# Performance work log

Measured on AMD Instinct MI355X. Metric: run time of the kernel, lower is better.

## Reference

```python
import jax, jax.numpy as jnp
import numpy as np

DIVERSITY_WEIGHT = 0.3
UNCERTAINTY_WEIGHT = 0.3
EPS_NORM = 1e-12  # torch F.normalize eps
EPS_LOG = 1e-8


def setup_inputs() -> dict:
    key = jax.random.key(0)
    k1, k2 = jax.random.split(key)
    B, N, D, C = 8, 8192, 512, 2
    x = jax.random.normal(k1, (B, N, D), dtype=jnp.float32)
    c = jax.random.normal(k2, (B, N, C), dtype=jnp.float32)
    return {"x": x, "c": c, "big_lambda": 512}


def reference(x, c, big_lambda):
    B, N, D = x.shape
    C = c.shape[-1]
    big_lambda = min(big_lambda, N)

    # relevance: max class score per instance (C > 1 branch)
    if C == 1:
        relevance = c[..., 0]
    else:
        relevance = jnp.max(c, axis=-1)  # [B, N]

    # diversity: 1 - mean cosine similarity to all other patches.
    # Row-sum of the N x N cosine-sim matrix factorizes:
    #   sum_j xn_i . xn_j = xn_i . (sum_j xn_j)  -> O(N*D) instead of O(N^2*D)
    norms = jnp.linalg.norm(x, axis=-1, keepdims=True)
    x_norm = x / jnp.maximum(norms, EPS_NORM)          # [B, N, D]
    s = jnp.sum(x_norm, axis=1)                        # [B, D]
    row_sums = jnp.einsum('bnd,bd->bn', x_norm, s)     # [B, N]
    avg_sim = (row_sums - 1.0) / (N - 1)
    diversity = 1.0 - avg_sim

    # uncertainty: entropy of class distribution
    if C == 1:
        p = jax.nn.sigmoid(c[..., 0])
        probs = jnp.stack([1.0 - p, p], axis=-1)
    else:
        probs = jax.nn.softmax(c, axis=-1)
    uncertainty = -jnp.sum(probs * jnp.log(probs + EPS_LOG), axis=-1)  # [B, N]

    combined = relevance + DIVERSITY_WEIGHT * diversity + UNCERTAINTY_WEIGHT * uncertainty

    _, selected_indices = jax.lax.top_k(combined, big_lambda)  # [B, big_lambda]
    attention_weights = jax.nn.softmax(combined, axis=1)       # [B, N]
    return selected_indices, attention_weights
```

## Files before the change

### kernel.cpp

```cpp
#include <hip/hip_runtime.h>
#include <stdint.h>

#define B 8
#define N 8192
#define D 512
#define K 512
#define DIV_W 0.3f
#define UNC_W 0.3f

constexpr int ROWS_PER_WAVE  = 16;
constexpr int WAVES_PER_BLK  = 4;
constexpr int ROWS_PER_BLOCK = ROWS_PER_WAVE * WAVES_PER_BLK;
constexpr int BLOCKS_PER_B   = N / ROWS_PER_BLOCK;

constexpr float DIVC = DIV_W * (1.0f + 1.0f / 8191.0f);
constexpr float COEF = DIV_W / 8191.0f;

__device__ __forceinline__ uint32_t ordmap(float f) {
    uint32_t u = __float_as_uint(f);
    return (u & 0x80000000u) ? ~u : (u | 0x80000000u);
}
__device__ __forceinline__ float ordunmap(uint32_t u) {
    return (u >> 31) ? __uint_as_float(u & 0x7FFFFFFFu) : __uint_as_float(~u);
}

__global__ __launch_bounds__(256) void k_norm_s(const float* __restrict__ x,
                                                const float* __restrict__ c,
                                                float* __restrict__ inv_norm,
                                                float* __restrict__ partials,
                                                float* __restrict__ combined) {
    int blk  = blockIdx.x;
    int b    = blk / BLOCKS_PER_B;
    int rb   = (blk % BLOCKS_PER_B) * ROWS_PER_BLOCK;
    int tid  = threadIdx.x;
    int wave = tid >> 6;
    int lane = tid & 63;

    const float4* xb = (const float4*)(x + (size_t)b * N * D);

    float4 accA = {0.f, 0.f, 0.f, 0.f};
    float4 accB = {0.f, 0.f, 0.f, 0.f};

    int row0 = rb + wave * ROWS_PER_WAVE;
    #pragma unroll 4
    for (int r = 0; r < ROWS_PER_WAVE; ++r) {
        int row = row0 + r;
        const float4* xr = xb + (size_t)row * (D / 4);
        float4 a  = xr[lane];
        float4 bb = xr[64 + lane];

        float ss = a.x*a.x + a.y*a.y + a.z*a.z + a.w*a.w
                 + bb.x*bb.x + bb.y*bb.y + bb.z*bb.z + bb.w*bb.w;
        #pragma unroll
        for (int o = 32; o > 0; o >>= 1) ss += __shfl_xor(ss, o, 64);

        float inv = 1.0f / fmaxf(sqrtf(ss), 1e-12f);
        if (lane == 0) inv_norm[b * N + row] = inv;

        accA.x += a.x * inv;  accA.y += a.y * inv;
        accA.z += a.z * inv;  accA.w += a.w * inv;
        accB.x += bb.x * inv; accB.y += bb.y * inv;
        accB.z += bb.z * inv; accB.w += bb.w * inv;
    }

    if (lane < 16) {
        int row = row0 + lane;
        float2 cv = ((const float2*)c)[(size_t)b * N + row];
        float rel = fmaxf(cv.x, cv.y);
        float e0 = expf(cv.x - rel), e1 = expf(cv.y - rel);
        float Z  = e0 + e1;
        float p0 = e0 / Z, p1 = e1 / Z;
        float ent = -(p0 * logf(p0 + 1e-8f) + p1 * logf(p1 + 1e-8f));
        combined[b * N + row] = rel + UNC_W * ent + DIVC;
    }

    __shared__ float sp[WAVES_PER_BLK][D];
    float* dA = &sp[wave][lane * 4];
    dA[0] = accA.x; dA[1] = accA.y; dA[2] = accA.z; dA[3] = accA.w;
    float* dB = &sp[wave][256 + lane * 4];
    dB[0] = accB.x; dB[1] = accB.y; dB[2] = accB.z; dB[3] = accB.w;
    __syncthreads();

    float* dst = partials + (size_t)blk * D;
    for (int d = tid; d < D; d += 256)
        dst[d] = sp[0][d] + sp[1][d] + sp[2][d] + sp[3][d];
}

__global__ __launch_bounds__(512) void k_reduce_s(const float* __restrict__ partials,
                                                  float* __restrict__ s) {
    int b = blockIdx.x;
    int d = threadIdx.x;
    const float* p = partials + (size_t)b * BLOCKS_PER_B * D + d;
    float acc = 0.f;
    #pragma unroll 16
    for (int j = 0; j < BLOCKS_PER_B; ++j) acc += p[(size_t)j * D];
    s[b * D + d] = acc;
}

__global__ __launch_bounds__(256) void k_combined(const float* __restrict__ x,
                                                  const float* __restrict__ inv_norm,
                                                  const float* __restrict__ s,
                                                  float* __restrict__ combined) {
    __shared__ float sl[D];
    int blk  = blockIdx.x;
    int b    = blk / BLOCKS_PER_B;
    int rb   = (blk % BLOCKS_PER_B) * ROWS_PER_BLOCK;
    int tid  = threadIdx.x;
    int wave = tid >> 6;
    int lane = tid & 63;

    for (int d = tid; d < D; d += 256) sl[d] = s[b * D + d];
    __syncthreads();

    const float4* sv = (const float4*)sl;
    float4 sA = sv[lane];
    float4 sB = sv[64 + lane];

    const float4* xb = (const float4*)(x + (size_t)b * N * D);
    int row0 = rb + wave * ROWS_PER_WAVE;
    #pragma unroll 4
    for (int r = 0; r < ROWS_PER_WAVE; ++r) {
        int row = row0 + r;
        const float4* xr = xb + (size_t)row * (D / 4);
        float4 a  = xr[lane];
        float4 bb = xr[64 + lane];

        float dot = a.x*sA.x + a.y*sA.y + a.z*sA.z + a.w*sA.w
                  + bb.x*sB.x + bb.y*sB.y + bb.z*sB.z + bb.w*sB.w;
        #pragma unroll
        for (int o = 32; o > 0; o >>= 1) dot += __shfl_xor(dot, o, 64);

        if (lane == 0) {
            float rs = dot * inv_norm[b * N + row];
            combined[b * N + row] -= COEF * rs;
        }
    }
}

struct P3 {
    unsigned long long cand[K];
    uint32_t hist[256];
    uint32_t tiew[256];
    uint16_t rnk[2][K];
    uint32_t wred[16];
    float    fred[16];
    uint32_t sc_prefix, sc_remK, sc_cnt;
};

__global__ __launch_bounds__(1024) void k_topk_sm(const float* __restrict__ combined,
                                                  float* __restrict__ out_idx,
                                                  float* __restrict__ out_w) {
    __shared__ P3 p3;

    const int b    = blockIdx.x;
    const int tid  = threadIdx.x;
    const int lane = tid & 63;
    const int wave = tid >> 6;

    const float4* cb4 = (const float4*)(combined + b * N);
    float4 f0 = cb4[tid];
    float4 f1 = cb4[1024 + tid];

    uint32_t v[8];
    v[0] = ordmap(f0.x); v[1] = ordmap(f0.y); v[2] = ordmap(f0.z); v[3] = ordmap(f0.w);
    v[4] = ordmap(f1.x); v[5] = ordmap(f1.y); v[6] = ordmap(f1.z); v[7] = ordmap(f1.w);

    uint32_t umax = 0;
    #pragma unroll
    for (int q = 0; q < 8; ++q) umax = max(umax, v[q]);
    #pragma unroll
    for (int o = 32; o > 0; o >>= 1) umax = max(umax, __shfl_xor(umax, o, 64));
    if (lane == 0) p3.wred[wave] = umax;
    if (tid == 0) { p3.sc_remK = K; p3.sc_prefix = 0u; p3.sc_cnt = 0u; }
    __syncthreads();
    uint32_t bmax = p3.wred[0];
    #pragma unroll
    for (int q = 1; q < 16; ++q) bmax = max(bmax, p3.wred[q]);
    const float m = ordunmap(bmax);

    float e[8];
    float sum = 0.f;
    #pragma unroll
    for (int q = 0; q < 8; ++q) { e[q] = expf(ordunmap(v[q]) - m); sum += e[q]; }
    #pragma unroll
    for (int o = 32; o > 0; o >>= 1) sum += __shfl_xor(sum, o, 64);
    if (lane == 0) p3.fred[wave] = sum;
    __syncthreads();
    float Z = 0.f;
    #pragma unroll
    for (int q = 0; q < 16; ++q) Z += p3.fred[q];
    const float invZ = 1.0f / Z;
    float4* ow = (float4*)(out_w + b * N);
    float4 w0 = {e[0]*invZ, e[1]*invZ, e[2]*invZ, e[3]*invZ};
    float4 w1 = {e[4]*invZ, e[5]*invZ, e[6]*invZ, e[7]*invZ};
    ow[tid]        = w0;
    ow[1024 + tid] = w1;

    uint32_t prefix = 0, maskHi = 0;
    for (int p = 3; p >= 0; --p) {
        if (tid < 256) p3.hist[tid] = 0u;
        __syncthreads();
        const int sh = 8 * p;
        if (p == 3) {
            #pragma unroll
            for (int q = 0; q < 8; ++q) {
                uint32_t bin = v[q] >> 24;
                bool pred = true;
                unsigned long long todo = ~0ULL;
                while (todo) {
                    int leader = __ffsll(todo) - 1;
                    uint32_t lbin = __shfl(bin, leader, 64);
                    unsigned long long same = __ballot(pred && (bin == lbin));
                    if (lane == leader) atomicAdd(&p3.hist[lbin], (uint32_t)__popcll(same));
                    todo &= ~same;
                    if (bin == lbin) pred = false;
                }
            }
        } else {
            #pragma unroll
            for (int q = 0; q < 8; ++q) {
                if ((v[q] & maskHi) == prefix)
                    atomicAdd(&p3.hist[(v[q] >> sh) & 0xFFu], 1u);
            }
        }
        __syncthreads();
        if (wave == 0) {
            uint32_t cc[4], lsum = 0;
            #pragma unroll
            for (int q = 0; q < 4; ++q) { cc[q] = p3.hist[lane * 4 + q]; lsum += cc[q]; }
            uint32_t ssum = lsum;
            #pragma unroll
            for (int off = 1; off < 64; off <<= 1) {
                uint32_t t2 = __shfl_down(ssum, off, 64);
                if (lane + off < 64) ssum += t2;
            }
            uint32_t cum = ssum - lsum;
            const uint32_t remK = p3.sc_remK;
            #pragma unroll
            for (int q = 3; q >= 0; --q) {
                if (cum < remK && cum + cc[q] >= remK) {
                    p3.sc_prefix = prefix | ((uint32_t)(lane * 4 + q) << sh);
                    p3.sc_remK   = remK - cum;
                }
                cum += cc[q];
            }
        }
        __syncthreads();
        prefix = p3.sc_prefix;
        maskHi |= (0xFFu << sh);
    }
    const uint32_t T    = prefix;
    const uint32_t remF = p3.sc_remK;

    if (tid < 256) p3.tiew[tid] = 0u;
    __syncthreads();
    #pragma unroll
    for (int q = 0; q < 8; ++q) {
        uint32_t idx = (q < 4) ? (uint32_t)(4 * tid + q)
                               : (uint32_t)(4096 + 4 * tid + (q - 4));
        bool g = (v[q] > T);
        unsigned long long mask = __ballot(g);
        if (mask) {
            int leader = __ffsll(mask) - 1;
            uint32_t bcnt = (uint32_t)__popcll(mask);
            uint32_t wbase = 0;
            if (lane == leader) wbase = atomicAdd(&p3.sc_cnt, bcnt);
            wbase = __shfl(wbase, leader, 64);
            if (g) {
                uint32_t off = (uint32_t)__popcll(mask & ((1ULL << lane) - 1ULL));
                p3.cand[wbase + off] = ((uint64_t)v[q] << 13) | (uint32_t)(8191 - idx);
            }
        }
        if (v[q] == T) atomicOr(&p3.tiew[idx >> 5], 1u << (idx & 31));
    }
    __syncthreads();
    const uint32_t base = p3.sc_cnt;
    if (wave == 0) {
        const int w0i = lane * 4;
        uint32_t lsum = 0;
        #pragma unroll
        for (int q = 0; q < 4; ++q) lsum += __popc(p3.tiew[w0i + q]);
        uint32_t ssum = lsum;
        #pragma unroll
        for (int off = 1; off < 64; off <<= 1) {
            uint32_t t2 = __shfl_up(ssum, off, 64);
            if (lane >= off) ssum += t2;
        }
        uint32_t rank = ssum - lsum;
        for (int q = 0; q < 4; ++q) {
            uint32_t word = p3.tiew[w0i + q];
            while (word) {
                int bpos = __builtin_ctz(word);
                if (rank < remF) {
                    uint32_t idx = (uint32_t)(w0i + q) * 32u + (uint32_t)bpos;
                    p3.cand[base + rank] = ((uint64_t)T << 13) | (uint32_t)(8191 - idx);
                }
                rank++;
                word &= word - 1;
            }
        }
    }
    __syncthreads();

    {
        const int ki   = tid & 511;
        const int half = tid >> 9;
        const uint64_t me = p3.cand[ki];
        const int j0 = half * 256;
        uint32_t cnt = 0;
        #pragma unroll 8
        for (int j = 0; j < 256; ++j)
            cnt += (p3.cand[j0 + j] > me) ? 1u : 0u;
        p3.rnk[half][ki] = (uint16_t)cnt;
    }
    __syncthreads();
    if (tid < K) {
        uint32_t rank = (uint32_t)p3.rnk[0][tid] + (uint32_t)p3.rnk[1][tid];
        uint32_t idx  = 8191u - (uint32_t)(p3.cand[tid] & 0x1FFFu);
        out_idx[b * K + rank] = (float)idx;
    }
}

extern "C" void kernel_launch(void* const* d_in, const int* in_sizes, int n_in,
                              void* d_out, int out_size, void* d_ws, size_t ws_size,
                              hipStream_t stream) {
    const float* x = (const float*)d_in[0];
    const float* c = (const float*)d_in[1];

    float* ws       = (float*)d_ws;
    float* partials = ws;
    float* s        = partials + B * BLOCKS_PER_B * D;
    float* inv_norm = s + B * D;
    float* combined = inv_norm + B * N;

    float* out = (float*)d_out;

    k_norm_s  <<<B * BLOCKS_PER_B, 256, 0, stream>>>(x, c, inv_norm, partials, combined);
    k_reduce_s<<<B, 512, 0, stream>>>(partials, s);
    k_combined<<<B * BLOCKS_PER_B, 256, 0, stream>>>(x, inv_norm, s, combined);
    k_topk_sm <<<B, 1024, 0, stream>>>(combined, out, out + B * K);
}
```

Before: 81.31 us.

## Replace partial-sum reduce kernel with atomics and rank-count with bitonic sort

Each norm block now adds its per-block column sums into s with atomicAdd, which removes the separate k_reduce_s launch and the partials buffer, but adds a memset. In the top-k kernel, the O(K^2) rank counting over candidates is replaced by a 512-element bitonic sort that uses shuffles for small strides and shared memory for large ones. The softmax exponent also switches to __expf. Float atomics make the accumulation order nondeterministic, and __expf gives slightly less precise weights.

```diff
diff --git a/kernel.cpp b/kernel.cpp
--- a/kernel.cpp
+++ b/kernel.cpp
@@ -27,7 +27,7 @@
 __global__ __launch_bounds__(256) void k_norm_s(const float* __restrict__ x,
                                                 const float* __restrict__ c,
                                                 float* __restrict__ inv_norm,
-                                                float* __restrict__ partials,
+                                                float* __restrict__ s,
                                                 float* __restrict__ combined) {
     int blk  = blockIdx.x;
     int b    = blk / BLOCKS_PER_B;
@@ -81,20 +81,10 @@
     dB[0] = accB.x; dB[1] = accB.y; dB[2] = accB.z; dB[3] = accB.w;
     __syncthreads();
 
-    float* dst = partials + (size_t)blk * D;
-    for (int d = tid; d < D; d += 256)
-        dst[d] = sp[0][d] + sp[1][d] + sp[2][d] + sp[3][d];
-}
-
-__global__ __launch_bounds__(512) void k_reduce_s(const float* __restrict__ partials,
-                                                  float* __restrict__ s) {
-    int b = blockIdx.x;
-    int d = threadIdx.x;
-    const float* p = partials + (size_t)b * BLOCKS_PER_B * D + d;
-    float acc = 0.f;
-    #pragma unroll 16
-    for (int j = 0; j < BLOCKS_PER_B; ++j) acc += p[(size_t)j * D];
-    s[b * D + d] = acc;
+    for (int d = tid; d < D; d += 256) {
+        float v = sp[0][d] + sp[1][d] + sp[2][d] + sp[3][d];
+        atomicAdd(&s[b * D + d], v);
+    }
 }
 
 __global__ __launch_bounds__(256) void k_combined(const float* __restrict__ x,
@@ -141,7 +131,6 @@
     unsigned long long cand[K];
     uint32_t hist[256];
     uint32_t tiew[256];
-    uint16_t rnk[2][K];
     uint32_t wred[16];
     float    fred[16];
     uint32_t sc_prefix, sc_remK, sc_cnt;
@@ -181,7 +170,7 @@
     float e[8];
     float sum = 0.f;
     #pragma unroll
-    for (int q = 0; q < 8; ++q) { e[q] = expf(ordunmap(v[q]) - m); sum += e[q]; }
+    for (int q = 0; q < 8; ++q) { e[q] = __expf(ordunmap(v[q]) - m); sum += e[q]; }
     #pragma unroll
     for (int o = 32; o > 0; o >>= 1) sum += __shfl_xor(sum, o, 64);
     if (lane == 0) p3.fred[wave] = sum;
@@ -302,23 +291,27 @@
     }
     __syncthreads();
 
-    {
-        const int ki   = tid & 511;
-        const int half = tid >> 9;
-        const uint64_t me = p3.cand[ki];
-        const int j0 = half * 256;
-        uint32_t cnt = 0;
-        #pragma unroll 8
-        for (int j = 0; j < 256; ++j)
-            cnt += (p3.cand[j0 + j] > me) ? 1u : 0u;
-        p3.rnk[half][ki] = (uint16_t)cnt;
-    }
-    __syncthreads();
-    if (tid < K) {
-        uint32_t rank = (uint32_t)p3.rnk[0][tid] + (uint32_t)p3.rnk[1][tid];
-        uint32_t idx  = 8191u - (uint32_t)(p3.cand[tid] & 0x1FFFu);
-        out_idx[b * K + rank] = (float)idx;
-    }
+    uint64_t sv = (tid < K) ? p3.cand[tid] : 0ULL;
+    __syncthreads();
+    for (int k = 2; k <= K; k <<= 1) {
+        for (int j = k >> 1; j > 0; j >>= 1) {
+            const bool desc  = ((tid & k) == 0);
+            const bool lower = ((tid & j) == 0);
+            uint64_t pv;
+            if (j >= 64) {
+                if (tid < K) p3.cand[tid] = sv;
+                __syncthreads();
+                pv = (tid < K) ? p3.cand[tid ^ j] : 0ULL;
+                __syncthreads();
+            } else {
+                pv = __shfl_xor(sv, j, 64);
+            }
+            const bool keepmax = (lower == desc);
+            if (tid < K && (keepmax ? (pv > sv) : (pv < sv))) sv = pv;
+        }
+    }
+    if (tid < K)
+        out_idx[b * K + tid] = (float)(8191u - (uint32_t)(sv & 0x1FFFu));
 }
 
 extern "C" void kernel_launch(void* const* d_in, const int* in_sizes, int n_in,
@@ -328,15 +321,14 @@
     const float* c = (const float*)d_in[1];
 
     float* ws       = (float*)d_ws;
-    float* partials = ws;
-    float* s        = partials + B * BLOCKS_PER_B * D;
+    float* s        = ws;
     float* inv_norm = s + B * D;
     float* combined = inv_norm + B * N;
 
     float* out = (float*)d_out;
 
-    k_norm_s  <<<B * BLOCKS_PER_B, 256, 0, stream>>>(x, c, inv_norm, partials, combined);
-    k_reduce_s<<<B, 512, 0, stream>>>(partials, s);
+    hipMemsetAsync(s, 0, B * D * sizeof(float), stream);
+    k_norm_s  <<<B * BLOCKS_PER_B, 256, 0, stream>>>(x, c, inv_norm, s, combined);
     k_combined<<<B * BLOCKS_PER_B, 256, 0, stream>>>(x, inv_norm, s, combined);
     k_topk_sm <<<B, 1024, 0, stream>>>(combined, out, out + B * K);
 }
```

New measurement: 79.73 us. Within noise of the previous version (-1.9%).
